# Performance work log

Measured on AMD Instinct MI355X. Metric: run time of the kernel, lower is better.

The kernel has to match this reference:

```python
import jax, jax.numpy as jnp
import numpy as np

N_NODES = 100000
N_EDGES = 600000
N_GRAPHS = 512
F_IN = 128
F_HID = 128
F_OUT = 128


def setup_inputs() -> dict:
    key = jax.random.key(0)
    ks = jax.random.split(key, 10)
    x = jax.random.normal(ks[0], (N_NODES, F_IN), dtype=jnp.float32)
    edge_index = jax.random.randint(ks[1], (2, N_EDGES), 0, N_NODES, dtype=jnp.int64)
    batch = jnp.sort(jax.random.randint(ks[2], (N_NODES,), 0, N_GRAPHS, dtype=jnp.int64))
    s1 = 1.0 / np.sqrt(F_IN)
    s2 = 1.0 / np.sqrt(F_HID)
    s3 = 1.0 / np.sqrt(F_OUT)
    W1 = jax.random.uniform(ks[3], (F_IN, F_HID), jnp.float32, -s1, s1)
    b1 = jnp.zeros((F_HID,), jnp.float32)
    W2 = jax.random.uniform(ks[4], (F_HID, F_OUT), jnp.float32, -s2, s2)
    b2 = jnp.zeros((F_OUT,), jnp.float32)
    Wlin = jax.random.uniform(ks[5], (F_OUT, 1), jnp.float32, -s3, s3)
    blin = jax.random.uniform(ks[6], (1,), jnp.float32, -s3, s3)
    return {"x": x, "edge_index": edge_index, "batch": batch,
            "W1": W1, "b1": b1, "W2": W2, "b2": b2, "Wlin": Wlin, "blin": blin}


def reference(x, edge_index, batch, W1, b1, W2, b2, Wlin, blin):
    N = x.shape[0]
    # GCN normalization with self-loops: D^{-1/2} (A + I) D^{-1/2}
    loop = jnp.arange(N, dtype=edge_index.dtype)
    src = jnp.concatenate([edge_index[0], loop])  # [E + N]
    dst = jnp.concatenate([edge_index[1], loop])
    deg = jax.ops.segment_sum(jnp.ones_like(dst, dtype=x.dtype), dst, num_segments=N)
    dis = jnp.where(deg > 0, jax.lax.rsqrt(jnp.maximum(deg, 1.0)), 0.0)  # deg^{-1/2}
    norm = (dis[src] * dis[dst])[:, None]  # [E+N, 1] edge weights

    def gcn_conv(h, W, b):
        hW = h @ W                                      # [N, d_out]
        msgs = norm * hW[src]                           # gather + scale
        agg = jax.ops.segment_sum(msgs, dst, num_segments=N)  # scatter-add
        return agg + b

    h = jax.nn.relu(gcn_conv(x, W1, b1))
    h = gcn_conv(h, W2, b2)

    # global_mean_pool over graph ids
    counts = jax.ops.segment_sum(jnp.ones((N,), x.dtype), batch, num_segments=N_GRAPHS)
    pooled = jax.ops.segment_sum(h, batch, num_segments=N_GRAPHS)
    pooled = pooled / jnp.maximum(counts, 1.0)[:, None]  # [N_GRAPHS, F_OUT]

    # dropout is identity in eval mode
    return pooled @ Wlin + blin  # [N_GRAPHS, 1]
```

## Files before the change

kernel.cpp:

```cpp
#include <hip/hip_runtime.h>

#define F 128

typedef __bf16 bf16x8 __attribute__((ext_vector_type(8)));
typedef float f32x4 __attribute__((ext_vector_type(4)));

__global__ __launch_bounds__(256) void k_prep(const float* __restrict__ W1, const float* __restrict__ W2,
                                              const float* __restrict__ Wlin, const float* __restrict__ b2,
                                              const float* __restrict__ blin, const int* __restrict__ batch,
                                              __bf16* __restrict__ Bswz, float* __restrict__ w2l,
                                              float* __restrict__ cconst, int* __restrict__ gstart,
                                              int* __restrict__ histg, float* __restrict__ deg,
                                              int N, int G, int bG) {
    int bid = blockIdx.x;
    int tid = threadIdx.x;
    if (bid < 64) {
        int o = bid * 256 + tid;
        int j = o & 7, lane = (o >> 3) & 63, tc = o >> 9;
        int t = tc >> 3, c = tc & 7;
        int k = t * 32 + (lane >> 4) * 8 + j;
        int n = c * 16 + (lane & 15);
        Bswz[o] = (__bf16)W1[k * F + n];
    } else if (bid == 64) {
        __shared__ float sh[F];
        if (tid < F) {
            float s = 0.0f;
            for (int j = 0; j < F; j += 4) {
                float4 w = *(const float4*)&W2[tid * F + j];
                float4 l = *(const float4*)&Wlin[j];
                s += w.x * l.x + w.y * l.y + w.z * l.z + w.w * l.w;
            }
            w2l[tid] = s;
            sh[tid] = b2[tid] * Wlin[tid];
        } else if (tid < F + 64) {
            histg[tid - F] = 0;
        }
        __syncthreads();
        if (tid == 0) {
            float c = blin[0];
            for (int j = 0; j < F; ++j) c += sh[j];
            *cconst = c;
        }
    } else if (bid < 65 + bG) {
        int g = (bid - 65) * 256 + tid;
        if (g < G) {
            int lo = 0, hi = N;
            while (lo < hi) { int mid = (lo + hi) >> 1; if (batch[mid] < g) lo = mid + 1; else hi = mid; }
            gstart[g] = lo;
            if (g == 0) gstart[G] = N;
        }
    } else {
        int i = (bid - 65 - bG) * 256 + tid;
        if (i < N) deg[i] = 1.0f;
    }
}

__global__ __launch_bounds__(256) void k_count(const int* __restrict__ dst, float* deg, int E) {
    int i = blockIdx.x * 256 + threadIdx.x;
    if (i < E) unsafeAtomicAdd(&deg[dst[i]], 1.0f);
}

__global__ __launch_bounds__(256) void k_scan1(const float* __restrict__ deg, int* __restrict__ pref,
                                               int* __restrict__ bsum, float* __restrict__ dis,
                                               int* __restrict__ histg, int N) {
    int t = threadIdx.x;
    __shared__ int lh[64];
    __shared__ int wtot[4];
    if (t < 64) lh[t] = 0;
    int base = blockIdx.x * 1024 + t * 4;
    int v[4]; int s = 0;
#pragma unroll
    for (int j = 0; j < 4; ++j) {
        int idx = base + j;
        float dv = (idx < N) ? deg[idx] : 1.0f;
        if (idx < N) dis[idx] = rsqrtf(dv);
        v[j] = (idx < N) ? ((int)dv - 1) : 0; s += v[j];
    }
    int lane = t & 63, w = t >> 6;
    int inc = s;
#pragma unroll
    for (int d = 1; d < 64; d <<= 1) { int o = __shfl_up(inc, d); if (lane >= d) inc += o; }
    if (lane == 63) wtot[w] = inc;
    __syncthreads();
#pragma unroll
    for (int j = 0; j < 4; ++j)
        if (base + j < N) atomicAdd(&lh[min(v[j], 63)], 1);
    int woff = 0;
#pragma unroll
    for (int i = 0; i < 4; ++i) if (i < w) woff += wtot[i];
    int run = woff + inc - s;
#pragma unroll
    for (int j = 0; j < 4; ++j) { int idx = base + j; if (idx < N) pref[idx] = run; run += v[j]; }
    if (t == 255) bsum[blockIdx.x] = woff + inc;
    __syncthreads();
    if (t < 64 && lh[t] > 0) atomicAdd(&histg[t], lh[t]);
}

__global__ __launch_bounds__(256) void k_scan3(int* __restrict__ pref, const int* __restrict__ bsum,
                                               int* __restrict__ cursor, const int* __restrict__ histg,
                                               int* __restrict__ bcur, int N, int E) {
    int t = threadIdx.x;
    int chunk = blockIdx.x >> 2;
    int partial = 0;
    for (int i = t; i < chunk; i += 256) partial += bsum[i];
    int lane = t & 63, w = t >> 6;
#pragma unroll
    for (int d = 1; d < 64; d <<= 1) partial += __shfl_xor(partial, d);
    __shared__ int ws4[4];
    if (lane == 0) ws4[w] = partial;
    __syncthreads();
    int off = ws4[0] + ws4[1] + ws4[2] + ws4[3];
    int i = blockIdx.x * 256 + t;
    if (i < N) {
        int v = pref[i] + off;
        pref[i] = v;
        cursor[i] = v;
    }
    if (i == 0) pref[N] = E;
    if (blockIdx.x == 0 && t < 64) {
        int h = histg[t];
        int inc2 = h;
#pragma unroll
        for (int d = 1; d < 64; d <<= 1) { int o = __shfl_up(inc2, d); if (t >= d) inc2 += o; }
        bcur[t] = inc2 - h;
    }
}

__global__ __launch_bounds__(256) void k_fill(const int* __restrict__ src, const int* __restrict__ dst,
                                              const float* __restrict__ deg, int* __restrict__ cursor,
                                              int* __restrict__ srcs, int* __restrict__ bcur,
                                              int* __restrict__ perm, int E, int N, int nbN) {
    int bid = blockIdx.x, tid = threadIdx.x;
    if (bid < nbN) {
        __shared__ int lcnt[64], lbase[64];
        if (tid < 64) lcnt[tid] = 0;
        __syncthreads();
        int n = bid * 256 + tid;
        int b = 0, r = 0;
        if (n < N) {
            b = min((int)deg[n] - 1, 63);
            r = atomicAdd(&lcnt[b], 1);
        }
        __syncthreads();
        if (tid < 64 && lcnt[tid] > 0) lbase[tid] = atomicAdd(&bcur[tid], lcnt[tid]);
        __syncthreads();
        if (n < N) perm[lbase[b] + r] = n;
    } else {
        int e = (bid - nbN) * 256 + tid;
        if (e < E) {
            int s = src[e], d = dst[e];
            int slot = atomicAdd(&cursor[d], 1);
            srcs[slot] = s;
        }
    }
}

__global__ __launch_bounds__(256) void k_gemm_mfma(const float* __restrict__ X,
                                                   const __bf16* __restrict__ Bswz,
                                                   const float* __restrict__ dis,
                                                   __bf16* __restrict__ Yb, int N) {
    int lane = threadIdx.x & 63, wave = threadIdx.x >> 6;
    int quad = lane >> 4, m = lane & 15;
    int r0 = blockIdx.x * 128 + wave * 32;

    f32x4 acc[2][8];
#pragma unroll
    for (int rt = 0; rt < 2; ++rt)
#pragma unroll
        for (int c = 0; c < 8; ++c) acc[rt][c] = (f32x4)0.0f;

    int ra = r0 + m;      if (ra >= N) ra = N - 1;
    int rb = r0 + 16 + m; if (rb >= N) rb = N - 1;
    const float* pxa = &X[(size_t)ra * F + quad * 8];
    const float* pxb = &X[(size_t)rb * F + quad * 8];

    float4 a0 = *(const float4*)pxa, a1 = *(const float4*)(pxa + 4);
    float4 a2 = *(const float4*)pxb, a3 = *(const float4*)(pxb + 4);

#pragma unroll 1
    for (int t = 0; t < 4; ++t) {
        const __bf16* bp = Bswz + (size_t)t * 4096 + lane * 8;
        bf16x8 B[8];
#pragma unroll
        for (int c = 0; c < 8; ++c) B[c] = *(const bf16x8*)(bp + c * 512);

        float fa[8] = {a0.x, a0.y, a0.z, a0.w, a1.x, a1.y, a1.z, a1.w};
        float fb[8] = {a2.x, a2.y, a2.z, a2.w, a3.x, a3.y, a3.z, a3.w};
        bf16x8 ah0, al0, ah1, al1;
#pragma unroll
        for (int j = 0; j < 8; ++j) {
            __bf16 h0 = (__bf16)fa[j]; ah0[j] = h0; al0[j] = (__bf16)(fa[j] - (float)h0);
            __bf16 h1 = (__bf16)fb[j]; ah1[j] = h1; al1[j] = (__bf16)(fb[j] - (float)h1);
        }
        if (t < 3) {
            a0 = *(const float4*)(pxa + (t + 1) * 32);
            a1 = *(const float4*)(pxa + (t + 1) * 32 + 4);
            a2 = *(const float4*)(pxb + (t + 1) * 32);
            a3 = *(const float4*)(pxb + (t + 1) * 32 + 4);
        }
#pragma unroll
        for (int c = 0; c < 8; ++c) {
            acc[0][c] = __builtin_amdgcn_mfma_f32_16x16x32_bf16(ah0, B[c], acc[0][c], 0, 0, 0);
            acc[0][c] = __builtin_amdgcn_mfma_f32_16x16x32_bf16(al0, B[c], acc[0][c], 0, 0, 0);
            acc[1][c] = __builtin_amdgcn_mfma_f32_16x16x32_bf16(ah1, B[c], acc[1][c], 0, 0, 0);
            acc[1][c] = __builtin_amdgcn_mfma_f32_16x16x32_bf16(al1, B[c], acc[1][c], 0, 0, 0);
        }
    }

#pragma unroll
    for (int rt = 0; rt < 2; ++rt) {
        int rbase = r0 + rt * 16 + quad * 4;
#pragma unroll
        for (int r = 0; r < 4; ++r) {
            int row = rbase + r;
            if (row < N) {
                float dr = dis[row];
#pragma unroll
                for (int c = 0; c < 8; ++c)
                    Yb[(size_t)row * F + c * 16 + m] = (__bf16)(acc[rt][c][r] * dr);
            }
        }
    }
}

__global__ __launch_bounds__(256) void k_agg_z(const __bf16* __restrict__ hWb, const float* __restrict__ dis,
                                               const int* __restrict__ rowptr, const int* __restrict__ srcs,
                                               const int* __restrict__ perm,
                                               const float* __restrict__ bias, const float* __restrict__ w2l,
                                               float* __restrict__ zt, int N) {
    int idx = blockIdx.x * 32 + (threadIdx.x >> 3);
    if (idx >= N) return;
    int node = perm[idx];
    int lane = threadIdx.x & 7;
    float di = dis[node];
    float s[16];
    {
        const __bf16* pr = &hWb[(size_t)node * F + lane * 16];
        bf16x8 v0 = *(const bf16x8*)pr;
        bf16x8 v1 = *(const bf16x8*)(pr + 8);
#pragma unroll
        for (int j = 0; j < 8; ++j) { s[j] = (float)v0[j]; s[8 + j] = (float)v1[j]; }
    }
    int e0 = rowptr[node], e1 = rowptr[node + 1];
    int e = e0;
    for (; e + 4 <= e1; e += 4) {
        int i0 = srcs[e], i1 = srcs[e + 1], i2 = srcs[e + 2], i3 = srcs[e + 3];
        const __bf16* p0 = &hWb[(size_t)i0 * F + lane * 16];
        const __bf16* p1 = &hWb[(size_t)i1 * F + lane * 16];
        const __bf16* p2 = &hWb[(size_t)i2 * F + lane * 16];
        const __bf16* p3 = &hWb[(size_t)i3 * F + lane * 16];
        bf16x8 a0 = *(const bf16x8*)p0, b0 = *(const bf16x8*)(p0 + 8);
        bf16x8 a1 = *(const bf16x8*)p1, b1 = *(const bf16x8*)(p1 + 8);
        bf16x8 a2 = *(const bf16x8*)p2, b2 = *(const bf16x8*)(p2 + 8);
        bf16x8 a3 = *(const bf16x8*)p3, b3 = *(const bf16x8*)(p3 + 8);
#pragma unroll
        for (int j = 0; j < 8; ++j) {
            s[j]     += (float)a0[j] + (float)a1[j] + (float)a2[j] + (float)a3[j];
            s[8 + j] += (float)b0[j] + (float)b1[j] + (float)b2[j] + (float)b3[j];
        }
    }
    for (; e < e1; ++e) {
        const __bf16* pr = &hWb[(size_t)srcs[e] * F + lane * 16];
        bf16x8 v0 = *(const bf16x8*)pr;
        bf16x8 v1 = *(const bf16x8*)(pr + 8);
#pragma unroll
        for (int j = 0; j < 8; ++j) { s[j] += (float)v0[j]; s[8 + j] += (float)v1[j]; }
    }
    float p = 0.0f;
#pragma unroll
    for (int q = 0; q < 4; ++q) {
        float4 bb = *(const float4*)&bias[lane * 16 + q * 4];
        float4 ww = *(const float4*)&w2l[lane * 16 + q * 4];
        p += fmaxf(fmaf(di, s[q * 4 + 0], bb.x), 0.0f) * ww.x;
        p += fmaxf(fmaf(di, s[q * 4 + 1], bb.y), 0.0f) * ww.y;
        p += fmaxf(fmaf(di, s[q * 4 + 2], bb.z), 0.0f) * ww.z;
        p += fmaxf(fmaf(di, s[q * 4 + 3], bb.w), 0.0f) * ww.w;
    }
#pragma unroll
    for (int d = 1; d < 8; d <<= 1) p += __shfl_xor(p, d);
    if (lane == 0) zt[node] = di * p;
}

__global__ __launch_bounds__(256) void k_pool(const float* __restrict__ zt, const float* __restrict__ dis,
                                              const int* __restrict__ rowptr, const int* __restrict__ srcs,
                                              const int* __restrict__ gstart, const float* __restrict__ cconst,
                                              const float* __restrict__ blin, float* __restrict__ out, int G) {
    int g = blockIdx.x;
    int g0 = gstart[g], g1 = gstart[g + 1];
    float acc = 0.0f;
    for (int n = g0 + threadIdx.x; n < g1; n += 256) {
        float s = zt[n];
        int e0 = rowptr[n], e1 = rowptr[n + 1];
        int e = e0;
        for (; e + 4 <= e1; e += 4) {
            s += zt[srcs[e]] + zt[srcs[e + 1]] + zt[srcs[e + 2]] + zt[srcs[e + 3]];
        }
        for (; e < e1; ++e) s += zt[srcs[e]];
        acc += dis[n] * s;
    }
#pragma unroll
    for (int d = 1; d < 64; d <<= 1) acc += __shfl_xor(acc, d);
    __shared__ float ws4[4];
    if ((threadIdx.x & 63) == 0) ws4[threadIdx.x >> 6] = acc;
    __syncthreads();
    if (threadIdx.x == 0) {
        float sum = ws4[0] + ws4[1] + ws4[2] + ws4[3];
        int c = g1 - g0;
        out[g] = (c > 0) ? (sum / (float)c + cconst[0]) : blin[0];
    }
}


extern "C" void kernel_launch(void* const* d_in, const int* in_sizes, int n_in,
                              void* d_out, int out_size, void* d_ws, size_t ws_size,
                              hipStream_t stream) {
    const float* x    = (const float*)d_in[0];
    const int*   ei   = (const int*)d_in[1];
    const int*   batch= (const int*)d_in[2];
    const float* W1   = (const float*)d_in[3];
    const float* b1   = (const float*)d_in[4];
    const float* W2   = (const float*)d_in[5];
    const float* b2   = (const float*)d_in[6];
    const float* Wlin = (const float*)d_in[7];
    const float* blin = (const float*)d_in[8];
    float* out = (float*)d_out;

    const int N = in_sizes[2];
    const int E = in_sizes[1] / 2;
    const int G = out_size;
    const int* src = ei;
    const int* dst = ei + E;

    char* p = (char*)d_ws;
    auto take = [&](size_t bytes) { char* q = p; p += (bytes + 255) & ~(size_t)255; return q; };
    __bf16* hWb    = (__bf16*)take((size_t)N * F * 2);
    float*  ztbuf  = (float*)take((size_t)N * 4);
    float*  deg    = (float*)take((size_t)N * 4);
    float*  dis    = (float*)take((size_t)N * 4);
    int*    rowptr = (int*)  take((size_t)(N + 1) * 4);
    int*    cursor = (int*)  take((size_t)N * 4);
    int*    srcs   = (int*)  take((size_t)E * 4);
    int*    perm   = (int*)  take((size_t)N * 4);
    int*    bsum   = (int*)  take(4096);
    int*    histg  = (int*)  take(64 * 4);
    int*    bcur   = (int*)  take(64 * 4);
    int*    gstart = (int*)  take((size_t)(G + 1) * 4);
    float*  w2l    = (float*)take((size_t)F * 4);
    float*  cconst = (float*)take(256);
    __bf16* Bswz   = (__bf16*)take((size_t)F * F * 2);

    const int nbN = (N + 255) / 256;
    const int nbE = (E + 255) / 256;
    const int nbS = (N + 1023) / 1024;
    const int bG  = (G + 255) / 256;

    k_prep <<<65 + bG + nbN, 256, 0, stream>>>(W1, W2, Wlin, b2, blin, batch,
                                               Bswz, w2l, cconst, gstart, histg, deg, N, G, bG);
    k_count<<<nbE, 256, 0, stream>>>(dst, deg, E);
    k_scan1<<<nbS, 256, 0, stream>>>(deg, rowptr, bsum, dis, histg, N);
    k_scan3<<<nbN, 256, 0, stream>>>(rowptr, bsum, cursor, histg, bcur, N, E);
    k_fill <<<nbN + nbE, 256, 0, stream>>>(src, dst, deg, cursor, srcs, bcur, perm, E, N, nbN);

    k_gemm_mfma<<<(N + 127) / 128, 256, 0, stream>>>(x, Bswz, dis, hWb, N);
    k_agg_z<<<(N + 31) / 32, 256, 0, stream>>>(hWb, dis, rowptr, srcs, perm, b1, w2l, ztbuf, N);
    k_pool <<<G, 256, 0, stream>>>(ztbuf, dis, rowptr, srcs, gstart, cconst, blin, out, G);
}
```

Baseline: 221.0 us.

## Vectorize edge kernels, double-buffer GEMM loads, batch gather loads in aggregation

The edge-count and CSR-fill kernels now have each thread handle four edges through int4 loads, which cuts the launched block count by four. The GEMM prefetches two K-tiles of X ahead in a fully unrolled loop instead of one. The aggregation kernel gathers up to eight neighbour rows per batch, issuing all loads before accumulating, to raise memory-level parallelism. The costs are higher register pressure and fewer threads for the atomic-heavy kernels.

Measured after the change: 228.4 us. 1.03x slower.

```diff
diff --git a/kernel.cpp b/kernel.cpp
--- a/kernel.cpp
+++ b/kernel.cpp
@@ -56,8 +56,16 @@
 }
 
 __global__ __launch_bounds__(256) void k_count(const int* __restrict__ dst, float* deg, int E) {
-    int i = blockIdx.x * 256 + threadIdx.x;
-    if (i < E) unsafeAtomicAdd(&deg[dst[i]], 1.0f);
+    int base = (blockIdx.x * 256 + threadIdx.x) * 4;
+    if (base + 4 <= E) {
+        int4 d = *(const int4*)(dst + base);
+        unsafeAtomicAdd(&deg[d.x], 1.0f);
+        unsafeAtomicAdd(&deg[d.y], 1.0f);
+        unsafeAtomicAdd(&deg[d.z], 1.0f);
+        unsafeAtomicAdd(&deg[d.w], 1.0f);
+    } else {
+        for (int i = base; i < E; ++i) unsafeAtomicAdd(&deg[dst[i]], 1.0f);
+    }
 }
 
 __global__ __launch_bounds__(256) void k_scan1(const float* __restrict__ deg, int* __restrict__ pref,
@@ -146,11 +154,18 @@
         __syncthreads();
         if (n < N) perm[lbase[b] + r] = n;
     } else {
-        int e = (bid - nbN) * 256 + tid;
-        if (e < E) {
-            int s = src[e], d = dst[e];
-            int slot = atomicAdd(&cursor[d], 1);
-            srcs[slot] = s;
+        int base = ((bid - nbN) * 256 + tid) * 4;
+        if (base + 4 <= E) {
+            int4 s4 = *(const int4*)(src + base);
+            int4 d4 = *(const int4*)(dst + base);
+            srcs[atomicAdd(&cursor[d4.x], 1)] = s4.x;
+            srcs[atomicAdd(&cursor[d4.y], 1)] = s4.y;
+            srcs[atomicAdd(&cursor[d4.z], 1)] = s4.z;
+            srcs[atomicAdd(&cursor[d4.w], 1)] = s4.w;
+        } else {
+            for (int e = base; e < E; ++e) {
+                srcs[atomicAdd(&cursor[dst[e]], 1)] = src[e];
+            }
         }
     }
 }
@@ -174,29 +189,37 @@
     const float* pxa = &X[(size_t)ra * F + quad * 8];
     const float* pxb = &X[(size_t)rb * F + quad * 8];
 
-    float4 a0 = *(const float4*)pxa, a1 = *(const float4*)(pxa + 4);
-    float4 a2 = *(const float4*)pxb, a3 = *(const float4*)(pxb + 4);
-
-#pragma unroll 1
+    float4 a0[2], a1[2], a2[2], a3[2];
+#pragma unroll
+    for (int t = 0; t < 2; ++t) {
+        a0[t] = *(const float4*)(pxa + t * 32);
+        a1[t] = *(const float4*)(pxa + t * 32 + 4);
+        a2[t] = *(const float4*)(pxb + t * 32);
+        a3[t] = *(const float4*)(pxb + t * 32 + 4);
+    }
+
+#pragma unroll
     for (int t = 0; t < 4; ++t) {
+        int cur = t & 1;
+        float4 xa0 = a0[cur], xa1 = a1[cur], xa2 = a2[cur], xa3 = a3[cur];
+        if (t < 2) {
+            a0[cur] = *(const float4*)(pxa + (t + 2) * 32);
+            a1[cur] = *(const float4*)(pxa + (t + 2) * 32 + 4);
+            a2[cur] = *(const float4*)(pxb + (t + 2) * 32);
+            a3[cur] = *(const float4*)(pxb + (t + 2) * 32 + 4);
+        }
         const __bf16* bp = Bswz + (size_t)t * 4096 + lane * 8;
         bf16x8 B[8];
 #pragma unroll
         for (int c = 0; c < 8; ++c) B[c] = *(const bf16x8*)(bp + c * 512);
 
-        float fa[8] = {a0.x, a0.y, a0.z, a0.w, a1.x, a1.y, a1.z, a1.w};
-        float fb[8] = {a2.x, a2.y, a2.z, a2.w, a3.x, a3.y, a3.z, a3.w};
+        float fa[8] = {xa0.x, xa0.y, xa0.z, xa0.w, xa1.x, xa1.y, xa1.z, xa1.w};
+        float fb[8] = {xa2.x, xa2.y, xa2.z, xa2.w, xa3.x, xa3.y, xa3.z, xa3.w};
         bf16x8 ah0, al0, ah1, al1;
 #pragma unroll
         for (int j = 0; j < 8; ++j) {
             __bf16 h0 = (__bf16)fa[j]; ah0[j] = h0; al0[j] = (__bf16)(fa[j] - (float)h0);
             __bf16 h1 = (__bf16)fb[j]; ah1[j] = h1; al1[j] = (__bf16)(fb[j] - (float)h1);
-        }
-        if (t < 3) {
-            a0 = *(const float4*)(pxa + (t + 1) * 32);
-            a1 = *(const float4*)(pxa + (t + 1) * 32 + 4);
-            a2 = *(const float4*)(pxb + (t + 1) * 32);
-            a3 = *(const float4*)(pxb + (t + 1) * 32 + 4);
         }
 #pragma unroll
         for (int c = 0; c < 8; ++c) {
@@ -242,29 +265,31 @@
         for (int j = 0; j < 8; ++j) { s[j] = (float)v0[j]; s[8 + j] = (float)v1[j]; }
     }
     int e0 = rowptr[node], e1 = rowptr[node + 1];
-    int e = e0;
-    for (; e + 4 <= e1; e += 4) {
-        int i0 = srcs[e], i1 = srcs[e + 1], i2 = srcs[e + 2], i3 = srcs[e + 3];
-        const __bf16* p0 = &hWb[(size_t)i0 * F + lane * 16];
-        const __bf16* p1 = &hWb[(size_t)i1 * F + lane * 16];
-        const __bf16* p2 = &hWb[(size_t)i2 * F + lane * 16];
-        const __bf16* p3 = &hWb[(size_t)i3 * F + lane * 16];
-        bf16x8 a0 = *(const bf16x8*)p0, b0 = *(const bf16x8*)(p0 + 8);
-        bf16x8 a1 = *(const bf16x8*)p1, b1 = *(const bf16x8*)(p1 + 8);
-        bf16x8 a2 = *(const bf16x8*)p2, b2 = *(const bf16x8*)(p2 + 8);
-        bf16x8 a3 = *(const bf16x8*)p3, b3 = *(const bf16x8*)(p3 + 8);
-#pragma unroll
-        for (int j = 0; j < 8; ++j) {
-            s[j]     += (float)a0[j] + (float)a1[j] + (float)a2[j] + (float)a3[j];
-            s[8 + j] += (float)b0[j] + (float)b1[j] + (float)b2[j] + (float)b3[j];
-        }
-    }
-    for (; e < e1; ++e) {
-        const __bf16* pr = &hWb[(size_t)srcs[e] * F + lane * 16];
-        bf16x8 v0 = *(const bf16x8*)pr;
-        bf16x8 v1 = *(const bf16x8*)(pr + 8);
-#pragma unroll
-        for (int j = 0; j < 8; ++j) { s[j] += (float)v0[j]; s[8 + j] += (float)v1[j]; }
+    for (int e = e0; e < e1; ) {
+        int k = e1 - e; if (k > 8) k = 8;
+        int id[8];
+#pragma unroll
+        for (int i = 0; i < 8; ++i) if (i < k) id[i] = srcs[e + i];
+        bf16x8 va[8], vb[8];
+#pragma unroll
+        for (int i = 0; i < 8; ++i) {
+            if (i < k) {
+                const __bf16* p = &hWb[(size_t)id[i] * F + lane * 16];
+                va[i] = *(const bf16x8*)p;
+                vb[i] = *(const bf16x8*)(p + 8);
+            }
+        }
+#pragma unroll
+        for (int i = 0; i < 8; ++i) {
+            if (i < k) {
+#pragma unroll
+                for (int j = 0; j < 8; ++j) {
+                    s[j]     += (float)va[i][j];
+                    s[8 + j] += (float)vb[i][j];
+                }
+            }
+        }
+        e += k;
     }
     float p = 0.0f;
 #pragma unroll
@@ -349,17 +374,17 @@
     float*  cconst = (float*)take(256);
     __bf16* Bswz   = (__bf16*)take((size_t)F * F * 2);
 
-    const int nbN = (N + 255) / 256;
-    const int nbE = (E + 255) / 256;
-    const int nbS = (N + 1023) / 1024;
-    const int bG  = (G + 255) / 256;
+    const int nbN  = (N + 255) / 256;
+    const int nbE4 = (E + 1023) / 1024;
+    const int nbS  = (N + 1023) / 1024;
+    const int bG   = (G + 255) / 256;
 
     k_prep <<<65 + bG + nbN, 256, 0, stream>>>(W1, W2, Wlin, b2, blin, batch,
                                                Bswz, w2l, cconst, gstart, histg, deg, N, G, bG);
-    k_count<<<nbE, 256, 0, stream>>>(dst, deg, E);
+    k_count<<<nbE4, 256, 0, stream>>>(dst, deg, E);
     k_scan1<<<nbS, 256, 0, stream>>>(deg, rowptr, bsum, dis, histg, N);
     k_scan3<<<nbN, 256, 0, stream>>>(rowptr, bsum, cursor, histg, bcur, N, E);
-    k_fill <<<nbN + nbE, 256, 0, stream>>>(src, dst, deg, cursor, srcs, bcur, perm, E, N, nbN);
+    k_fill <<<nbN + nbE4, 256, 0, stream>>>(src, dst, deg, cursor, srcs, bcur, perm, E, N, nbN);
 
     k_gemm_mfma<<<(N + 127) / 128, 256, 0, stream>>>(x, Bswz, dis, hWb, N);
     k_agg_z<<<(N + 31) / 32, 256, 0, stream>>>(hWb, dis, rowptr, srcs, perm, b1, w2l, ztbuf, N);
```
